# Optimization experiments

Hardware: AMD Instinct MI355X
Metric: run time of the kernel (lower is better)

The kernel has to match this reference:

```python
import jax, jax.numpy as jnp
import numpy as np

NUM_HEADS = 16
NUM_KV_HEADS = 4
HEAD_DIM = 128
WINDOW = 1024
ROPE_BASE = 10000.0


def _rope_tables(seq_len, dtype):
    inv_freq = 1.0 / (ROPE_BASE ** (jnp.arange(0, HEAD_DIM, 2, dtype=jnp.float32) / HEAD_DIM))
    t = jnp.arange(seq_len, dtype=jnp.float32)
    freqs = t[:, None] * inv_freq[None, :]            # [S, hd/2]
    emb = jnp.concatenate([freqs, freqs], axis=-1)    # [S, hd]
    return jnp.cos(emb).astype(dtype), jnp.sin(emb).astype(dtype)


def _rotate_half(x):
    x1, x2 = jnp.split(x, 2, axis=-1)
    return jnp.concatenate([-x2, x1], axis=-1)


def _apply_rope(x, cos, sin):
    # x: [B, h, S, hd]; cos/sin: [S, hd]
    return x * cos[None, None, :, :] + _rotate_half(x) * sin[None, None, :, :]


def setup_inputs() -> dict:
    key = jax.random.key(0)
    ks = jax.random.split(key, 5)
    B, S, H = 2, 2048, 2048
    KV = NUM_KV_HEADS * HEAD_DIM
    return {
        "hidden_states": jax.random.normal(ks[0], (B, S, H), dtype=jnp.float32),
        "Wq": jax.random.normal(ks[1], (H, H), dtype=jnp.float32) * 0.02,
        "Wk": jax.random.normal(ks[2], (H, KV), dtype=jnp.float32) * 0.02,
        "Wv": jax.random.normal(ks[3], (H, KV), dtype=jnp.float32) * 0.02,
        "Wo": jax.random.normal(ks[4], (H, H), dtype=jnp.float32) * 0.02,
    }


def reference(hidden_states, Wq, Wk, Wv, Wo):
    B, S, H = hidden_states.shape
    G = NUM_HEADS // NUM_KV_HEADS

    q = (hidden_states @ Wq).reshape(B, S, NUM_HEADS, HEAD_DIM).transpose(0, 2, 1, 3)
    k = (hidden_states @ Wk).reshape(B, S, NUM_KV_HEADS, HEAD_DIM).transpose(0, 2, 1, 3)
    v = (hidden_states @ Wv).reshape(B, S, NUM_KV_HEADS, HEAD_DIM).transpose(0, 2, 1, 3)

    cos, sin = _rope_tables(S, hidden_states.dtype)
    q = _apply_rope(q, cos, sin)
    k = _apply_rope(k, cos, sin)

    # GQA without materializing repeated KV: group Q heads over KV heads.
    qg = q.reshape(B, NUM_KV_HEADS, G, S, HEAD_DIM)
    scale = 1.0 / jnp.sqrt(jnp.asarray(HEAD_DIM, hidden_states.dtype))
    scores = jnp.einsum("bgnqd,bgkd->bgnqk", qg, k) * scale  # [B, kvh, G, S, S]

    pos = jnp.arange(S)
    dist = pos[:, None] - pos[None, :]                 # q_pos - k_pos
    masked = (dist > WINDOW) | (dist < 0)              # sliding window + causal
    scores = jnp.where(masked[None, None, None, :, :], jnp.asarray(-jnp.inf, scores.dtype), scores)

    probs = jax.nn.softmax(scores, axis=-1)
    out = jnp.einsum("bgnqk,bgkd->bgnqd", probs, v)    # [B, kvh, G, S, hd]
    out = out.reshape(B, NUM_HEADS, S, HEAD_DIM).transpose(0, 2, 1, 3).reshape(B, S, H)
    return out @ Wo
```

## Files before the change

kernel.cpp:

```cpp
#include <hip/hip_runtime.h>
#include <math.h>

namespace {

typedef short s16;
typedef short s16x8 __attribute__((ext_vector_type(8)));
typedef float f32x4 __attribute__((ext_vector_type(4)));

constexpr int B   = 2;
constexpr int S   = 2048;
constexpr int H   = 2048;
constexpr int NH  = 16;
constexpr int NKV = 4;
constexpr int HD  = 128;
constexpr int WIN = 1024;
constexpr int M   = B * S;

__device__ inline s16 f2bs(float x) {
    unsigned u = __float_as_uint(x);
    u += 0x7fffu + ((u >> 16) & 1u);
    return (s16)(u >> 16);
}
__device__ inline float bs2f(s16 v) {
    return __uint_as_float(((unsigned)(unsigned short)v) << 16);
}

__device__ inline void gload_lds16(const void* g, void* l) {
    __builtin_amdgcn_global_load_lds(
        (const __attribute__((address_space(1))) void*)g,
        (__attribute__((address_space(3))) void*)l, 16, 0, 0);
}

__global__ __launch_bounds__(256) void cast_kernel(const float* __restrict__ X,
                                                   s16* __restrict__ Y, int n8) {
    int i = blockIdx.x * 256 + threadIdx.x;
    if (i >= n8) return;
    const float4* p = (const float4*)X + (size_t)i * 2;
    float4 a = p[0], b = p[1];
    s16x8 v;
    v[0] = f2bs(a.x); v[1] = f2bs(a.y); v[2] = f2bs(a.z); v[3] = f2bs(a.w);
    v[4] = f2bs(b.x); v[5] = f2bs(b.y); v[6] = f2bs(b.z); v[7] = f2bs(b.w);
    *(s16x8*)(Y + (size_t)i * 8) = v;
}

__global__ __launch_bounds__(256) void transpose_cast(const float* __restrict__ W,
                                                      s16* __restrict__ WT,
                                                      int K, int N) {
    __shared__ float tile[64][65];
    int c = threadIdx.x & 63, r4 = threadIdx.x >> 6;
    int nb = blockIdx.x * 64, kb = blockIdx.y * 64;
    #pragma unroll
    for (int i = 0; i < 16; ++i) {
        int r = r4 + i * 4;
        tile[r][c] = W[(size_t)(kb + r) * N + nb + c];
    }
    __syncthreads();
    #pragma unroll
    for (int i = 0; i < 16; ++i) {
        int r = r4 + i * 4;
        WT[(size_t)(nb + r) * K + kb + c] = f2bs(tile[c][r]);
    }
}

template <bool BF16OUT>
__global__ __launch_bounds__(256) void gemm_bf16(const s16* __restrict__ A,
                                                 const s16* __restrict__ BT,
                                                 void* __restrict__ Cv,
                                                 int Ndim, int Kdim) {
    __shared__ __align__(16) s16 As[128 * 32];
    __shared__ __align__(16) s16 Bs[128 * 32];

    const int t    = threadIdx.x;
    const int lane = t & 63;
    const int wid  = t >> 6;
    const int wr   = wid >> 1;
    const int wc   = wid & 1;
    const int rowBase = blockIdx.y * 128;
    const int colBase = blockIdx.x * 128;

    const s16* Ab = A  + (size_t)rowBase * Kdim;
    const s16* Bb = BT + (size_t)colBase * Kdim;

    f32x4 acc[4][4];
    #pragma unroll
    for (int m = 0; m < 4; ++m)
        #pragma unroll
        for (int n = 0; n < 4; ++n)
            acc[m][n] = (f32x4)0.f;

    for (int k0 = 0; k0 < Kdim; k0 += 32) {
        #pragma unroll
        for (int i = 0; i < 2; ++i) {
            int lc = i * 256 + t;
            int sr = lc >> 3;
            int cc = (lc & 7) ^ (sr & 7);
            int r  = (sr << 1) | (cc >> 2);
            int kg = cc & 3;
            const s16* ga = Ab + (size_t)r * Kdim + k0 + kg * 8;
            const s16* gb = Bb + (size_t)r * Kdim + k0 + kg * 8;
            char* la = (char*)As + i * 4096 + wid * 1024;
            char* lb = (char*)Bs + i * 4096 + wid * 1024;
            gload_lds16(ga, la);
            gload_lds16(gb, lb);
        }
        __syncthreads();

        s16x8 af[4], bfr[4];
        #pragma unroll
        for (int m = 0; m < 4; ++m) {
            int r  = wr * 64 + m * 16 + (lane & 15);
            int sr = r >> 1;
            int c  = ((r & 1) << 2) | (lane >> 4);
            int cs = c ^ (sr & 7);
            af[m] = *(const s16x8*)(As + sr * 64 + cs * 8);
        }
        #pragma unroll
        for (int n = 0; n < 4; ++n) {
            int r  = wc * 64 + n * 16 + (lane & 15);
            int sr = r >> 1;
            int c  = ((r & 1) << 2) | (lane >> 4);
            int cs = c ^ (sr & 7);
            bfr[n] = *(const s16x8*)(Bs + sr * 64 + cs * 8);
        }
        #pragma unroll
        for (int m = 0; m < 4; ++m)
            #pragma unroll
            for (int n = 0; n < 4; ++n)
                acc[m][n] = __builtin_amdgcn_mfma_f32_16x16x32_bf16(af[m], bfr[n], acc[m][n], 0, 0, 0);

        __syncthreads();
    }

    #pragma unroll
    for (int m = 0; m < 4; ++m) {
        int row = rowBase + wr * 64 + m * 16 + ((lane >> 4) << 2);
        #pragma unroll
        for (int n = 0; n < 4; ++n) {
            int col = colBase + wc * 64 + n * 16 + (lane & 15);
            if (BF16OUT) {
                s16* cp = (s16*)Cv + (size_t)row * Ndim + col;
                #pragma unroll
                for (int j = 0; j < 4; ++j)
                    cp[(size_t)j * Ndim] = f2bs(acc[m][n][j]);
            } else {
                float* cp = (float*)Cv + (size_t)row * Ndim + col;
                #pragma unroll
                for (int j = 0; j < 4; ++j)
                    cp[(size_t)j * Ndim] = acc[m][n][j];
            }
        }
    }
}

__global__ __launch_bounds__(256) void rope_kernel(s16* __restrict__ X, int nHmask,
                                                   int rowShift, int rowStride,
                                                   float scale, int total) {
    int idx = blockIdx.x * 256 + threadIdx.x;
    if (idx >= total) return;
    int jc  = idx & 7;
    int hh  = (idx >> 3) & nHmask;
    int row = idx >> rowShift;
    int s   = row & (S - 1);

    s16* base = X + (size_t)row * rowStride + hh * HD;
    s16x8 a = *(const s16x8*)(base + jc * 8);
    s16x8 b = *(const s16x8*)(base + 64 + jc * 8);
    s16x8 na, nb;
    #pragma unroll
    for (int i = 0; i < 8; ++i) {
        int j = jc * 8 + i;
        float f = (float)s * exp2f(-(float)j * 0.2076205059302203f);
        float sn, c;
        __sincosf(f, &sn, &c);
        float x1 = bs2f(a[i]), x2 = bs2f(b[i]);
        na[i] = f2bs((x1 * c - x2 * sn) * scale);
        nb[i] = f2bs((x2 * c + x1 * sn) * scale);
    }
    *(s16x8*)(base + jc * 8) = na;
    *(s16x8*)(base + 64 + jc * 8) = nb;
}

__global__ __launch_bounds__(256) void vtrans(const s16* __restrict__ KVb,
                                              s16* __restrict__ VT) {
    __shared__ s16 tl[64][72];
    const int t  = threadIdx.x;
    const int c8 = (t & 7) * 8;
    const int r  = t >> 3;
    const int s0 = blockIdx.x * 64;
    const int z  = blockIdx.y;
    const int bk = z >> 1;
    const int d0 = (z & 1) * 64;
    const int b  = bk >> 2, kvh = bk & 3;

    #pragma unroll
    for (int i = 0; i < 2; ++i) {
        int row = r + i * 32;
        *(s16x8*)&tl[row][c8] =
            *(const s16x8*)(KVb + (size_t)(b * S + s0 + row) * 1024 + 512 + kvh * HD + d0 + c8);
    }
    __syncthreads();
    #pragma unroll
    for (int i = 0; i < 2; ++i) {
        int drow = r + i * 32;
        s16x8 v;
        #pragma unroll
        for (int k = 0; k < 8; ++k) v[k] = tl[c8 + k][drow];
        *(s16x8*)(VT + (size_t)(bk * 128 + d0 + drow) * S + s0 + c8) = v;
    }
}

__global__ __launch_bounds__(256, 2) void attn_mfma(const s16* __restrict__ Q,
                                                    const s16* __restrict__ KV,
                                                    const s16* __restrict__ VT,
                                                    s16* __restrict__ O) {
    __shared__ __align__(16) s16 Kl[64 * 128];
    __shared__ __align__(16) s16 Vl[128 * 64];
    __shared__ __align__(16) s16 Pl[4][32 * 72];

    const int t    = threadIdx.x;
    const int lane = t & 63;
    const int wid  = t >> 6;
    const int g    = lane >> 4;
    const int cc   = lane & 15;
    const int bid  = blockIdx.x;
    const int qt   = bid & 63;
    const int kvh  = (bid >> 6) & 3;
    const int b    = bid >> 8;
    const int qbase = qt * 32;
    const int h    = kvh * 4 + wid;

    s16x8 qf[2][4];
    #pragma unroll
    for (int tq = 0; tq < 2; ++tq)
        #pragma unroll
        for (int kc = 0; kc < 4; ++kc)
            qf[tq][kc] = *(const s16x8*)(Q + (size_t)(b * S + qbase + tq * 16 + cc) * 2048
                                           + h * HD + kc * 32 + g * 8);

    float m_[2][4], l_[2][4];
    f32x4 o_[2][8];
    #pragma unroll
    for (int tq = 0; tq < 2; ++tq) {
        #pragma unroll
        for (int j = 0; j < 4; ++j) { m_[tq][j] = -1e30f; l_[tq][j] = 0.f; }
        #pragma unroll
        for (int dt = 0; dt < 8; ++dt) o_[tq][dt] = (f32x4)0.f;
    }

    const int kvstart = qbase >= WIN ? qbase - WIN : 0;
    const int nt = (qbase + 32 - kvstart + 63) >> 6;

    for (int it = 0; it < nt; ++it) {
        const int kvb = kvstart + it * 64;

        #pragma unroll
        for (int i = 0; i < 4; ++i) {
            int lc = i * 256 + t;
            {
                int r = lc >> 4, sl = lc & 15;
                int ch = sl ^ (r & 15);
                int kvr = kvb + r; if (kvr > S - 1) kvr = S - 1;
                gload_lds16(KV + (size_t)(b * S + kvr) * 1024 + kvh * HD + ch * 8,
                            (char*)Kl + i * 4096 + wid * 1024);
            }
            {
                int d = lc >> 3, sl = lc & 7;
                int ch = sl ^ (d & 7);
                int col = kvb + ch * 8; if (col > S - 8) col = S - 8;
                gload_lds16(VT + (size_t)((b * 4 + kvh) * HD + d) * S + col,
                            (char*)Vl + i * 4096 + wid * 1024);
            }
        }
        __syncthreads();

        f32x4 sv[2][4];
        #pragma unroll
        for (int tq = 0; tq < 2; ++tq)
            #pragma unroll
            for (int n = 0; n < 4; ++n) sv[tq][n] = (f32x4)0.f;
        #pragma unroll
        for (int n = 0; n < 4; ++n) {
            int r = n * 16 + cc;
            #pragma unroll
            for (int kc = 0; kc < 4; ++kc) {
                int sl = (kc * 4 + g) ^ (r & 15);
                s16x8 kf = *(const s16x8*)(Kl + r * 128 + sl * 8);
                sv[0][n] = __builtin_amdgcn_mfma_f32_16x16x32_bf16(qf[0][kc], kf, sv[0][n], 0, 0, 0);
                sv[1][n] = __builtin_amdgcn_mfma_f32_16x16x32_bf16(qf[1][kc], kf, sv[1][n], 0, 0, 0);
            }
        }

        if (kvb + 63 > qbase || kvb < qbase + 31 - WIN) {
            #pragma unroll
            for (int tq = 0; tq < 2; ++tq)
                #pragma unroll
                for (int j = 0; j < 4; ++j) {
                    int qp = qbase + tq * 16 + 4 * g + j;
                    #pragma unroll
                    for (int n = 0; n < 4; ++n) {
                        int dist = qp - (kvb + n * 16 + cc);
                        if (!(dist >= 0 && dist <= WIN)) sv[tq][n][j] = -1e30f;
                    }
                }
        }

        #pragma unroll
        for (int tq = 0; tq < 2; ++tq) {
            float mx4[4];
            bool need = false;
            #pragma unroll
            for (int j = 0; j < 4; ++j) {
                float mx = fmaxf(fmaxf(sv[tq][0][j], sv[tq][1][j]),
                                 fmaxf(sv[tq][2][j], sv[tq][3][j]));
                #pragma unroll
                for (int off = 1; off < 16; off <<= 1) mx = fmaxf(mx, __shfl_xor(mx, off));
                mx4[j] = mx;
                need |= (mx > m_[tq][j] + 8.f);
            }
            if (__ballot(need) != 0ull) {
                #pragma unroll
                for (int j = 0; j < 4; ++j) {
                    float mn = fmaxf(m_[tq][j], mx4[j]);
                    float a  = __expf(m_[tq][j] - mn);
                    m_[tq][j] = mn;
                    l_[tq][j] *= a;
                    #pragma unroll
                    for (int dt = 0; dt < 8; ++dt) o_[tq][dt][j] *= a;
                }
            }
            #pragma unroll
            for (int j = 0; j < 4; ++j) {
                int row = tq * 16 + 4 * g + j;
                float ps = 0.f;
                #pragma unroll
                for (int n = 0; n < 4; ++n) {
                    float pv = __expf(sv[tq][n][j] - m_[tq][j]);
                    ps += pv;
                    Pl[wid][row * 72 + n * 16 + cc] = f2bs(pv);
                }
                #pragma unroll
                for (int off = 1; off < 16; off <<= 1) ps += __shfl_xor(ps, off);
                l_[tq][j] += ps;
            }
        }

        #pragma unroll
        for (int ks = 0; ks < 2; ++ks) {
            s16x8 pa0 = *(const s16x8*)(&Pl[wid][(0  + cc) * 72 + ks * 32 + g * 8]);
            s16x8 pa1 = *(const s16x8*)(&Pl[wid][(16 + cc) * 72 + ks * 32 + g * 8]);
            #pragma unroll
            for (int dt = 0; dt < 8; ++dt) {
                int d = dt * 16 + cc;
                int sl = (ks * 4 + g) ^ (d & 7);
                s16x8 vf = *(const s16x8*)(Vl + d * 64 + sl * 8);
                o_[0][dt] = __builtin_amdgcn_mfma_f32_16x16x32_bf16(pa0, vf, o_[0][dt], 0, 0, 0);
                o_[1][dt] = __builtin_amdgcn_mfma_f32_16x16x32_bf16(pa1, vf, o_[1][dt], 0, 0, 0);
            }
        }

        __syncthreads();
    }

    #pragma unroll
    for (int tq = 0; tq < 2; ++tq) {
        #pragma unroll
        for (int j = 0; j < 4; ++j) {
            float inv = 1.0f / l_[tq][j];
            size_t rb = (size_t)(b * S + qbase + tq * 16 + 4 * g + j) * 2048 + h * HD;
            #pragma unroll
            for (int dt = 0; dt < 8; ++dt)
                O[rb + dt * 16 + cc] = f2bs(o_[tq][dt][j] * inv);
        }
    }
}

}

extern "C" void kernel_launch(void* const* d_in, const int* in_sizes, int n_in,
                              void* d_out, int out_size, void* d_ws, size_t ws_size,
                              hipStream_t stream) {
    const float* hs = (const float*)d_in[0];
    const float* Wq = (const float*)d_in[1];
    const float* Wk = (const float*)d_in[2];
    const float* Wv = (const float*)d_in[3];
    const float* Wo = (const float*)d_in[4];
    float* out = (float*)d_out;

    char* p = (char*)d_ws;
    s16* hsb  = (s16*)p;  p += (size_t)M * 2048 * 2;
    s16* WqT  = (s16*)p;  p += (size_t)2048 * 2048 * 2;
    s16* WkvT = (s16*)p;  p += (size_t)1024 * 2048 * 2;
    s16* WoT  = (s16*)p;  p += (size_t)2048 * 2048 * 2;
    s16* Qb   = (s16*)p;  p += (size_t)M * 2048 * 2;
    s16* KVb  = (s16*)p;  p += (size_t)M * 1024 * 2;
    s16* VT   = (s16*)p;
    s16* AOb  = hsb;

    dim3 blk(256);
    const float qscale = 0.08838834764831845f;

    cast_kernel<<<(M * H / 8 + 255) / 256, blk, 0, stream>>>(hs, hsb, M * H / 8);
    transpose_cast<<<dim3(2048 / 64, 2048 / 64), blk, 0, stream>>>(Wq, WqT, 2048, 2048);
    transpose_cast<<<dim3(512 / 64, 2048 / 64), blk, 0, stream>>>(Wk, WkvT, 2048, 512);
    transpose_cast<<<dim3(512 / 64, 2048 / 64), blk, 0, stream>>>(Wv, WkvT + (size_t)512 * 2048, 2048, 512);
    transpose_cast<<<dim3(2048 / 64, 2048 / 64), blk, 0, stream>>>(Wo, WoT, 2048, 2048);

    gemm_bf16<true><<<dim3(2048 / 128, M / 128), blk, 0, stream>>>(hsb, WqT, Qb, 2048, 2048);
    gemm_bf16<true><<<dim3(1024 / 128, M / 128), blk, 0, stream>>>(hsb, WkvT, KVb, 1024, 2048);

    rope_kernel<<<(M * NH * 8) / 256, blk, 0, stream>>>(Qb, 15, 7, 2048, qscale, M * NH * 8);
    rope_kernel<<<(M * NKV * 8) / 256, blk, 0, stream>>>(KVb, 3, 5, 1024, 1.0f, M * NKV * 8);

    vtrans<<<dim3(S / 64, B * NKV * 2), blk, 0, stream>>>(KVb, VT);

    attn_mfma<<<B * NKV * (S / 32), blk, 0, stream>>>(Qb, KVb, VT, AOb);

    gemm_bf16<false><<<dim3(2048 / 128, M / 128), blk, 0, stream>>>(AOb, WoT, out, 2048, 2048);
}
```

Measured before the change: 360.7 us.

## Fuse QKV projections into one GEMM, widen K-tile, add XCD-aware block swizzle

Q, K and V projection weights are packed into one 3072-column transposed matrix, so a single GEMM writes a combined QKV buffer. The rope, vtrans and attention kernels now index into that buffer with a 3072-element row stride. The GEMM K-tile doubles from 32 to 64 with a new LDS swizzle and two MFMA sub-steps per barrier, halving the number of barriers. Workgroup IDs are remapped in groups of eight and occupancy is hinted at 2 blocks per CU. The aim is fewer launches, better tail utilisation and better L2 reuse, at the cost of doubled LDS per block.

Result: faster. 294.1 us (-18.5%).

```diff
diff --git a/kernel.cpp b/kernel.cpp
--- a/kernel.cpp
+++ b/kernel.cpp
@@ -15,6 +15,7 @@
 constexpr int HD  = 128;
 constexpr int WIN = 1024;
 constexpr int M   = B * S;
+constexpr int QKVN = 3072;
 
 __device__ inline s16 f2bs(float x) {
     unsigned u = __float_as_uint(x);
@@ -63,20 +64,25 @@
 }
 
 template <bool BF16OUT>
-__global__ __launch_bounds__(256) void gemm_bf16(const s16* __restrict__ A,
-                                                 const s16* __restrict__ BT,
-                                                 void* __restrict__ Cv,
-                                                 int Ndim, int Kdim) {
-    __shared__ __align__(16) s16 As[128 * 32];
-    __shared__ __align__(16) s16 Bs[128 * 32];
+__global__ __launch_bounds__(256, 2) void gemm_bf16(const s16* __restrict__ A,
+                                                    const s16* __restrict__ BT,
+                                                    void* __restrict__ Cv,
+                                                    int Ndim, int Kdim) {
+    __shared__ __align__(16) s16 As[128 * 64];
+    __shared__ __align__(16) s16 Bs[128 * 64];
 
     const int t    = threadIdx.x;
     const int lane = t & 63;
     const int wid  = t >> 6;
     const int wr   = wid >> 1;
     const int wc   = wid & 1;
-    const int rowBase = blockIdx.y * 128;
-    const int colBase = blockIdx.x * 128;
+
+    const int gx   = gridDim.x;
+    const int nwg  = gx * gridDim.y;
+    const int wgid = blockIdx.y * gx + blockIdx.x;
+    const int swz  = (wgid & 7) * (nwg >> 3) + (wgid >> 3);
+    const int rowBase = (swz / gx) * 128;
+    const int colBase = (swz % gx) * 128;
 
     const s16* Ab = A  + (size_t)rowBase * Kdim;
     const s16* Bb = BT + (size_t)colBase * Kdim;
@@ -88,45 +94,43 @@
         for (int n = 0; n < 4; ++n)
             acc[m][n] = (f32x4)0.f;
 
-    for (int k0 = 0; k0 < Kdim; k0 += 32) {
-        #pragma unroll
-        for (int i = 0; i < 2; ++i) {
+    for (int k0 = 0; k0 < Kdim; k0 += 64) {
+        #pragma unroll
+        for (int i = 0; i < 4; ++i) {
             int lc = i * 256 + t;
-            int sr = lc >> 3;
-            int cc = (lc & 7) ^ (sr & 7);
-            int r  = (sr << 1) | (cc >> 2);
-            int kg = cc & 3;
-            const s16* ga = Ab + (size_t)r * Kdim + k0 + kg * 8;
-            const s16* gb = Bb + (size_t)r * Kdim + k0 + kg * 8;
-            char* la = (char*)As + i * 4096 + wid * 1024;
-            char* lb = (char*)Bs + i * 4096 + wid * 1024;
-            gload_lds16(ga, la);
-            gload_lds16(gb, lb);
+            int r  = lc >> 3;
+            int sl = lc & 7;
+            int ch = sl ^ (r & 7);
+            const s16* ga = Ab + (size_t)r * Kdim + k0 + ch * 8;
+            const s16* gb = Bb + (size_t)r * Kdim + k0 + ch * 8;
+            gload_lds16(ga, (char*)As + i * 4096 + wid * 1024);
+            gload_lds16(gb, (char*)Bs + i * 4096 + wid * 1024);
         }
         __syncthreads();
 
-        s16x8 af[4], bfr[4];
-        #pragma unroll
-        for (int m = 0; m < 4; ++m) {
-            int r  = wr * 64 + m * 16 + (lane & 15);
-            int sr = r >> 1;
-            int c  = ((r & 1) << 2) | (lane >> 4);
-            int cs = c ^ (sr & 7);
-            af[m] = *(const s16x8*)(As + sr * 64 + cs * 8);
-        }
-        #pragma unroll
-        for (int n = 0; n < 4; ++n) {
-            int r  = wc * 64 + n * 16 + (lane & 15);
-            int sr = r >> 1;
-            int c  = ((r & 1) << 2) | (lane >> 4);
-            int cs = c ^ (sr & 7);
-            bfr[n] = *(const s16x8*)(Bs + sr * 64 + cs * 8);
-        }
-        #pragma unroll
-        for (int m = 0; m < 4; ++m)
-            #pragma unroll
-            for (int n = 0; n < 4; ++n)
-                acc[m][n] = __builtin_amdgcn_mfma_f32_16x16x32_bf16(af[m], bfr[n], acc[m][n], 0, 0, 0);
+        #pragma unroll
+        for (int kk = 0; kk < 2; ++kk) {
+            s16x8 af[4], bfr[4];
+            #pragma unroll
+            for (int m = 0; m < 4; ++m) {
+                int r  = wr * 64 + m * 16 + (lane & 15);
+                int c  = kk * 4 + (lane >> 4);
+                int cs = c ^ (r & 7);
+                af[m] = *(const s16x8*)(As + r * 64 + cs * 8);
+            }
+            #pragma unroll
+            for (int n = 0; n < 4; ++n) {
+                int r  = wc * 64 + n * 16 + (lane & 15);
+                int c  = kk * 4 + (lane >> 4);
+                int cs = c ^ (r & 7);
+                bfr[n] = *(const s16x8*)(Bs + r * 64 + cs * 8);
+            }
+            #pragma unroll
+            for (int m = 0; m < 4; ++m)
+                #pragma unroll
+                for (int n = 0; n < 4; ++n)
+                    acc[m][n] = __builtin_amdgcn_mfma_f32_16x16x32_bf16(af[m], bfr[n], acc[m][n], 0, 0, 0);
+        }
 
         __syncthreads();
     }
@@ -180,7 +184,7 @@
     *(s16x8*)(base + 64 + jc * 8) = nb;
 }
 
-__global__ __launch_bounds__(256) void vtrans(const s16* __restrict__ KVb,
+__global__ __launch_bounds__(256) void vtrans(const s16* __restrict__ VB,
                                               s16* __restrict__ VT) {
     __shared__ s16 tl[64][72];
     const int t  = threadIdx.x;
@@ -196,7 +200,7 @@
     for (int i = 0; i < 2; ++i) {
         int row = r + i * 32;
         *(s16x8*)&tl[row][c8] =
-            *(const s16x8*)(KVb + (size_t)(b * S + s0 + row) * 1024 + 512 + kvh * HD + d0 + c8);
+            *(const s16x8*)(VB + (size_t)(b * S + s0 + row) * QKVN + kvh * HD + d0 + c8);
     }
     __syncthreads();
     #pragma unroll
@@ -210,7 +214,7 @@
 }
 
 __global__ __launch_bounds__(256, 2) void attn_mfma(const s16* __restrict__ Q,
-                                                    const s16* __restrict__ KV,
+                                                    const s16* __restrict__ KB,
                                                     const s16* __restrict__ VT,
                                                     s16* __restrict__ O) {
     __shared__ __align__(16) s16 Kl[64 * 128];
@@ -234,7 +238,7 @@
     for (int tq = 0; tq < 2; ++tq)
         #pragma unroll
         for (int kc = 0; kc < 4; ++kc)
-            qf[tq][kc] = *(const s16x8*)(Q + (size_t)(b * S + qbase + tq * 16 + cc) * 2048
+            qf[tq][kc] = *(const s16x8*)(Q + (size_t)(b * S + qbase + tq * 16 + cc) * QKVN
                                            + h * HD + kc * 32 + g * 8);
 
     float m_[2][4], l_[2][4];
@@ -260,7 +264,7 @@
                 int r = lc >> 4, sl = lc & 15;
                 int ch = sl ^ (r & 15);
                 int kvr = kvb + r; if (kvr > S - 1) kvr = S - 1;
-                gload_lds16(KV + (size_t)(b * S + kvr) * 1024 + kvh * HD + ch * 8,
+                gload_lds16(KB + (size_t)(b * S + kvr) * QKVN + kvh * HD + ch * 8,
                             (char*)Kl + i * 4096 + wid * 1024);
             }
             {
@@ -387,33 +391,30 @@
     float* out = (float*)d_out;
 
     char* p = (char*)d_ws;
-    s16* hsb  = (s16*)p;  p += (size_t)M * 2048 * 2;
-    s16* WqT  = (s16*)p;  p += (size_t)2048 * 2048 * 2;
-    s16* WkvT = (s16*)p;  p += (size_t)1024 * 2048 * 2;
-    s16* WoT  = (s16*)p;  p += (size_t)2048 * 2048 * 2;
-    s16* Qb   = (s16*)p;  p += (size_t)M * 2048 * 2;
-    s16* KVb  = (s16*)p;  p += (size_t)M * 1024 * 2;
-    s16* VT   = (s16*)p;
-    s16* AOb  = hsb;
+    s16* hsb   = (s16*)p;  p += (size_t)M * 2048 * 2;
+    s16* WqkvT = (s16*)p;  p += (size_t)QKVN * 2048 * 2;
+    s16* WoT   = (s16*)p;  p += (size_t)2048 * 2048 * 2;
+    s16* QKVf  = (s16*)p;  p += (size_t)M * QKVN * 2;
+    s16* VT    = (s16*)p;
+    s16* AOb   = hsb;
 
     dim3 blk(256);
     const float qscale = 0.08838834764831845f;
 
     cast_kernel<<<(M * H / 8 + 255) / 256, blk, 0, stream>>>(hs, hsb, M * H / 8);
-    transpose_cast<<<dim3(2048 / 64, 2048 / 64), blk, 0, stream>>>(Wq, WqT, 2048, 2048);
-    transpose_cast<<<dim3(512 / 64, 2048 / 64), blk, 0, stream>>>(Wk, WkvT, 2048, 512);
-    transpose_cast<<<dim3(512 / 64, 2048 / 64), blk, 0, stream>>>(Wv, WkvT + (size_t)512 * 2048, 2048, 512);
+    transpose_cast<<<dim3(2048 / 64, 2048 / 64), blk, 0, stream>>>(Wq, WqkvT, 2048, 2048);
+    transpose_cast<<<dim3(512 / 64, 2048 / 64), blk, 0, stream>>>(Wk, WqkvT + (size_t)2048 * 2048, 2048, 512);
+    transpose_cast<<<dim3(512 / 64, 2048 / 64), blk, 0, stream>>>(Wv, WqkvT + (size_t)2560 * 2048, 2048, 512);
     transpose_cast<<<dim3(2048 / 64, 2048 / 64), blk, 0, stream>>>(Wo, WoT, 2048, 2048);
 
-    gemm_bf16<true><<<dim3(2048 / 128, M / 128), blk, 0, stream>>>(hsb, WqT, Qb, 2048, 2048);
-    gemm_bf16<true><<<dim3(1024 / 128, M / 128), blk, 0, stream>>>(hsb, WkvT, KVb, 1024, 2048);
-
-    rope_kernel<<<(M * NH * 8) / 256, blk, 0, stream>>>(Qb, 15, 7, 2048, qscale, M * NH * 8);
-    rope_kernel<<<(M * NKV * 8) / 256, blk, 0, stream>>>(KVb, 3, 5, 1024, 1.0f, M * NKV * 8);
-
-    vtrans<<<dim3(S / 64, B * NKV * 2), blk, 0, stream>>>(KVb, VT);
-
-    attn_mfma<<<B * NKV * (S / 32), blk, 0, stream>>>(Qb, KVb, VT, AOb);
+    gemm_bf16<true><<<dim3(QKVN / 128, M / 128), blk, 0, stream>>>(hsb, WqkvT, QKVf, QKVN, 2048);
+
+    rope_kernel<<<(M * NH * 8) / 256, blk, 0, stream>>>(QKVf, 15, 7, QKVN, qscale, M * NH * 8);
+    rope_kernel<<<(M * NKV * 8) / 256, blk, 0, stream>>>(QKVf + 2048, 3, 5, QKVN, 1.0f, M * NKV * 8);
+
+    vtrans<<<dim3(S / 64, B * NKV * 2), blk, 0, stream>>>(QKVf + 2560, VT);
+
+    attn_mfma<<<B * NKV * (S / 32), blk, 0, stream>>>(QKVf, QKVf + 2048, VT, AOb);
 
     gemm_bf16<false><<<dim3(2048 / 128, M / 128), blk, 0, stream>>>(AOb, WoT, out, 2048, 2048);
 }
```
